# Kernel optimization log

Measured on AMD Instinct MI355X. Metric: run time of the kernel, lower is better.

Reference implementation:

```python
import jax, jax.numpy as jnp
import numpy as np
import math

INPUT_SIZE = 2048
HIDDEN_SIZE = 2048
BATCH = 4096


def setup_inputs() -> dict:
    key = jax.random.key(0)
    ks = jax.random.split(key, 16)
    stdv = 1.0 / math.sqrt(HIDDEN_SIZE)

    def u(k, shape):
        return jax.random.uniform(k, shape, jnp.float32, -stdv, stdv)

    inp = {
        "x": jax.random.normal(ks[0], (BATCH, INPUT_SIZE), jnp.float32),
        "h_x": jax.random.normal(ks[1], (BATCH, HIDDEN_SIZE), jnp.float32),
        "c_x": jax.random.normal(ks[2], (BATCH, HIDDEN_SIZE), jnp.float32),
        "W_xi": u(ks[3], (INPUT_SIZE, HIDDEN_SIZE)),
        "W_hi": u(ks[4], (HIDDEN_SIZE, HIDDEN_SIZE)),
        "b_i": u(ks[5], (HIDDEN_SIZE,)),
        "W_xf": u(ks[6], (INPUT_SIZE, HIDDEN_SIZE)),
        "W_hf": u(ks[7], (HIDDEN_SIZE, HIDDEN_SIZE)),
        "b_f": u(ks[8], (HIDDEN_SIZE,)),
        "W_xc": u(ks[9], (INPUT_SIZE, HIDDEN_SIZE)),
        "W_hc": u(ks[10], (HIDDEN_SIZE, HIDDEN_SIZE)),
        "b_c": u(ks[11], (HIDDEN_SIZE,)),
        "W_xo": u(ks[12], (INPUT_SIZE, HIDDEN_SIZE)),
        "W_ho": u(ks[13], (HIDDEN_SIZE, HIDDEN_SIZE)),
        "b_o": u(ks[14], (HIDDEN_SIZE,)),
    }
    return inp


def reference(x, h_x, c_x, W_xi, W_hi, b_i, W_xf, W_hf, b_f, W_xc, W_hc, b_c, W_xo, W_ho, b_o):
    # LSTM cell: 4 gates, each x @ W_x* + h @ W_h* + b_*
    input_gate = jax.nn.sigmoid(x @ W_xi + h_x @ W_hi + b_i)
    forget_gate = jax.nn.sigmoid(x @ W_xf + h_x @ W_hf + b_f)
    output_gate = jax.nn.sigmoid(x @ W_xo + h_x @ W_ho + b_o)
    c_tilda = jnp.tanh(x @ W_xc + h_x @ W_hc + b_c)
    cy = forget_gate * c_x + input_gate * c_tilda
    hy = output_gate * jnp.tanh(cy)
    return (hy, cy)
```

## Files before the change

kernel.cpp:

```cpp
#include <hip/hip_runtime.h>
#include <stdint.h>

typedef __attribute__((ext_vector_type(8))) short short8;
typedef __attribute__((ext_vector_type(8))) unsigned short ushort8;
typedef __attribute__((ext_vector_type(4))) float floatx4;

#define BATCH 4096
#define HID   2048
#define KTOT  4096

__device__ __forceinline__ uint16_t f2bf(float f) {
    union { uint32_t i; float f; } v; v.f = f;
    uint32_t u = v.i;
    u += 0x7fffu + ((u >> 16) & 1u);
    return (uint16_t)(u >> 16);
}
__device__ __forceinline__ float sigmoid_f(float v) {
    return 1.0f / (1.0f + __expf(-v));
}
__device__ __forceinline__ float tanh_f(float v) {
    v = fminf(fmaxf(v, -15.0f), 15.0f);
    float e = __expf(-2.0f * v);
    return (1.0f - e) / (1.0f + e);
}
__device__ __forceinline__ void load_lds16(const uint16_t* g, uint16_t* l) {
    __builtin_amdgcn_global_load_lds(
        (const __attribute__((address_space(1))) void*)g,
        (__attribute__((address_space(3))) void*)l, 16, 0, 0);
}

__global__ __launch_bounds__(256) void conv_w(
    const float* __restrict__ w0, const float* __restrict__ w1,
    const float* __restrict__ w2, const float* __restrict__ w3,
    const float* __restrict__ w4, const float* __restrict__ w5,
    const float* __restrict__ w6, const float* __restrict__ w7,
    uint16_t* __restrict__ wt)
{
    int b   = blockIdx.x;
    int mi  = b >> 8;
    int rem = b & 255;
    int k0  = (rem >> 4) * 128;
    int n0  = (rem & 15) * 128;
    const float* src;
    switch (mi) {
        case 0: src = w0; break; case 1: src = w1; break;
        case 2: src = w2; break; case 3: src = w3; break;
        case 4: src = w4; break; case 5: src = w5; break;
        case 6: src = w6; break; default: src = w7; break;
    }
    int g = mi >> 1, half = mi & 1;
    int ty = threadIdx.x >> 4, tx = threadIdx.x & 15;
    int kr = k0 + ty * 8;
    int nc = n0 + tx * 8;

    ushort8 a[8];
    #pragma unroll
    for (int j = 0; j < 8; ++j) {
        const float* s = src + (size_t)(kr + j) * HID + nc;
        floatx4 f0 = *(const floatx4*)(s);
        floatx4 f1 = *(const floatx4*)(s + 4);
        #pragma unroll
        for (int i = 0; i < 4; ++i) {
            a[j][i]     = f2bf(f0[i]);
            a[j][4 + i] = f2bf(f1[i]);
        }
    }
    ushort8 bt[8];
    #pragma unroll
    for (int i = 0; i < 8; ++i)
        #pragma unroll
        for (int j = 0; j < 8; ++j)
            bt[i][j] = a[j][i];
    #pragma unroll
    for (int i = 0; i < 8; ++i)
        *(ushort8*)(wt + ((size_t)g * HID + nc + i) * KTOT + half * HID + kr) = bt[i];
}

__global__ __launch_bounds__(256) void conv_a(
    const float* __restrict__ x, const float* __restrict__ h,
    uint16_t* __restrict__ xh)
{
    size_t base = ((size_t)blockIdx.x * 256 + threadIdx.x) * 8;
    int m = (int)(base >> 12);
    int k = (int)(base & (KTOT - 1));
    const float* s = (k < HID) ? (x + (size_t)m * HID + k)
                               : (h + (size_t)m * HID + (k - HID));
    floatx4 f0 = *(const floatx4*)(s);
    floatx4 f1 = *(const floatx4*)(s + 4);
    ushort8 v;
    #pragma unroll
    for (int j = 0; j < 4; ++j) { v[j] = f2bf(f0[j]); v[4 + j] = f2bf(f1[j]); }
    *(ushort8*)(xh + base) = v;
}

__global__ __launch_bounds__(256, 4) void lstm_gemm_bf16(
    const uint16_t* __restrict__ xh, const float* __restrict__ cx,
    const uint16_t* __restrict__ wt,
    const float* __restrict__ bvi, const float* __restrict__ bvf,
    const float* __restrict__ bvo, const float* __restrict__ bvc,
    float* __restrict__ out)
{
    __shared__ uint16_t ldsA[128 * 64];
    __shared__ uint16_t ldsB[128 * 64];

    int t = threadIdx.x;
    int linear = blockIdx.y * gridDim.x + blockIdx.x;
    int my = (linear & 7) * 4 + ((linear >> 3) & 3);
    int nx = linear >> 5;
    int n0 = nx * 32;
    int m0 = my * 128;

    int wave = t >> 6, lane = t & 63;
    int wr = wave >> 1, wc = wave & 1;
    int lrow = lane & 15, quad = lane >> 4;
    int swz  = lrow & 7;

    int srow = t >> 3;
    int schk = (t & 7) ^ (srow & 7);

    floatx4 acc[4][4] = {};

    for (int kt = 0; kt < KTOT / 64; ++kt) {
        int k0 = kt * 64;

        __syncthreads();
        #pragma unroll
        for (int p = 0; p < 4; ++p) {
            int row = srow + p * 32;
            load_lds16(xh + (size_t)(m0 + row) * KTOT + k0 + schk * 8,
                       ldsA + p * 2048 + t * 8);
        }
        #pragma unroll
        for (int p = 0; p < 4; ++p) {
            int j = srow + p * 32;
            int g = j >> 5, dn = j & 31;
            load_lds16(wt + ((size_t)g * HID + n0 + dn) * KTOT + k0 + schk * 8,
                       ldsB + p * 2048 + t * 8);
        }
        __syncthreads();

        #pragma unroll
        for (int kh = 0; kh < 2; ++kh) {
            int kkc = kh * 4;
            short8 af[4], bfr[4];
            #pragma unroll
            for (int mi = 0; mi < 4; ++mi)
                af[mi] = *(const short8*)(ldsA + (wr * 64 + mi * 16 + lrow) * 64
                                               + (((quad + kkc) ^ swz)) * 8);
            #pragma unroll
            for (int g = 0; g < 4; ++g)
                bfr[g] = *(const short8*)(ldsB + (g * 32 + wc * 16 + lrow) * 64
                                               + (((quad + kkc) ^ swz)) * 8);
            #pragma unroll
            for (int mi = 0; mi < 4; ++mi)
                #pragma unroll
                for (int g = 0; g < 4; ++g)
                    acc[mi][g] = __builtin_amdgcn_mfma_f32_16x16x32_bf16(
                        af[mi], bfr[g], acc[mi][g], 0, 0, 0);
        }
    }

    int col = n0 + wc * 16 + lrow;
    float Bi = bvi[col], Bf = bvf[col], Bo = bvo[col], Bc = bvc[col];
    int rowb = m0 + wr * 64 + quad * 4;

    #pragma unroll
    for (int mi = 0; mi < 4; ++mi) {
        #pragma unroll
        for (int r = 0; r < 4; ++r) {
            int row = rowb + mi * 16 + r;
            size_t off = (size_t)row * HID + col;
            float gi = sigmoid_f(acc[mi][0][r] + Bi);
            float gf = sigmoid_f(acc[mi][1][r] + Bf);
            float go = sigmoid_f(acc[mi][2][r] + Bo);
            float gc = tanh_f   (acc[mi][3][r] + Bc);
            float cyv = gf * cx[off] + gi * gc;
            float hyv = go * tanh_f(cyv);
            out[off] = hyv;
            out[(size_t)BATCH * HID + off] = cyv;
        }
    }
}

__global__ __launch_bounds__(256) void lstm_fused_f32(
    const float* __restrict__ x, const float* __restrict__ h,
    const float* __restrict__ cx,
    const float* __restrict__ wxi, const float* __restrict__ whi,
    const float* __restrict__ wxf, const float* __restrict__ whf,
    const float* __restrict__ wxo, const float* __restrict__ who,
    const float* __restrict__ wxc, const float* __restrict__ whc,
    const float* __restrict__ bvi, const float* __restrict__ bvf,
    const float* __restrict__ bvo, const float* __restrict__ bvc,
    float* __restrict__ out)
{
    __shared__ uint16_t ldsA[128 * 32];
    __shared__ uint16_t ldsB[128 * 32];
    uint32_t* ldsB32 = (uint32_t*)ldsB;

    int t    = threadIdx.x;
    int n0   = blockIdx.x * 32;
    int m0   = blockIdx.y * 128;
    int wave = t >> 6, lane = t & 63;
    int wr = wave >> 1, wc = wave & 1;
    int lrow = lane & 15, quad = lane >> 4;
    int srow = t >> 2;
    int sseg = (t & 3) * 8;
    int gw = wave;
    int ng = lane & 3;
    int ka = lane >> 2;
    const float *wxg, *whg;
    switch (gw) {
        case 0:  wxg = wxi; whg = whi; break;
        case 1:  wxg = wxf; whg = whf; break;
        case 2:  wxg = wxo; whg = who; break;
        default: wxg = wxc; whg = whc; break;
    }

    floatx4 acc[4][4] = {};

    for (int kt = 0; kt < KTOT / 32; ++kt) {
        int k0  = kt * 32;
        int k0h = k0 & (HID - 1);
        bool xhalf = (k0 < HID);

        ushort8 va[2];
        uint32_t bw[8];
        const float* a = xhalf ? x : h;
        #pragma unroll
        for (int p = 0; p < 2; ++p) {
            const float* s = a + (size_t)(m0 + srow + p * 64) * HID + k0h + sseg;
            floatx4 f0 = *(const floatx4*)(s);
            floatx4 f1 = *(const floatx4*)(s + 4);
            #pragma unroll
            for (int j = 0; j < 4; ++j) {
                va[p][j]     = (short)f2bf(f0[j]);
                va[p][4 + j] = (short)f2bf(f1[j]);
            }
        }
        const float* wp  = xhalf ? wxg : whg;
        const float* r0p = wp + (size_t)(k0h + 2 * ka) * HID + n0 + ng * 8;
        floatx4 a0 = *(const floatx4*)(r0p);
        floatx4 a1 = *(const floatx4*)(r0p + 4);
        floatx4 b0 = *(const floatx4*)(r0p + HID);
        floatx4 b1 = *(const floatx4*)(r0p + HID + 4);
        #pragma unroll
        for (int j = 0; j < 4; ++j) {
            bw[j]     = (uint32_t)f2bf(a0[j]) | ((uint32_t)f2bf(b0[j]) << 16);
            bw[4 + j] = (uint32_t)f2bf(a1[j]) | ((uint32_t)f2bf(b1[j]) << 16);
        }

        __syncthreads();
        #pragma unroll
        for (int p = 0; p < 2; ++p)
            *(ushort8*)(ldsA + (srow + p * 64) * 32 + sseg) = va[p];
        #pragma unroll
        for (int j = 0; j < 8; ++j)
            ldsB32[(gw * 32 + ng * 8 + j) * 16 + ka] = bw[j];
        __syncthreads();

        short8 af[4], bfr[4];
        #pragma unroll
        for (int mi = 0; mi < 4; ++mi)
            af[mi] = *(const short8*)(ldsA + (wr * 64 + mi * 16 + lrow) * 32 + quad * 8);
        #pragma unroll
        for (int g = 0; g < 4; ++g)
            bfr[g] = *(const short8*)(ldsB + (g * 32 + wc * 16 + lrow) * 32 + quad * 8);

        #pragma unroll
        for (int mi = 0; mi < 4; ++mi)
            #pragma unroll
            for (int g = 0; g < 4; ++g)
                acc[mi][g] = __builtin_amdgcn_mfma_f32_16x16x32_bf16(
                    af[mi], bfr[g], acc[mi][g], 0, 0, 0);
    }

    int col = n0 + wc * 16 + lrow;
    float Bi = bvi[col], Bf = bvf[col], Bo = bvo[col], Bc = bvc[col];
    int rowb = m0 + wr * 64 + quad * 4;

    #pragma unroll
    for (int mi = 0; mi < 4; ++mi) {
        #pragma unroll
        for (int r = 0; r < 4; ++r) {
            int row = rowb + mi * 16 + r;
            size_t off = (size_t)row * HID + col;
            float gi = sigmoid_f(acc[mi][0][r] + Bi);
            float gf = sigmoid_f(acc[mi][1][r] + Bf);
            float go = sigmoid_f(acc[mi][2][r] + Bo);
            float gc = tanh_f   (acc[mi][3][r] + Bc);
            float cyv = gf * cx[off] + gi * gc;
            float hyv = go * tanh_f(cyv);
            out[off] = hyv;
            out[(size_t)BATCH * HID + off] = cyv;
        }
    }
}

extern "C" void kernel_launch(void* const* d_in, const int* in_sizes, int n_in,
                              void* d_out, int out_size, void* d_ws, size_t ws_size,
                              hipStream_t stream) {
    const float* x    = (const float*)d_in[0];
    const float* h_x  = (const float*)d_in[1];
    const float* c_x  = (const float*)d_in[2];
    const float* W_xi = (const float*)d_in[3];
    const float* W_hi = (const float*)d_in[4];
    const float* b_i  = (const float*)d_in[5];
    const float* W_xf = (const float*)d_in[6];
    const float* W_hf = (const float*)d_in[7];
    const float* b_f  = (const float*)d_in[8];
    const float* W_xc = (const float*)d_in[9];
    const float* W_hc = (const float*)d_in[10];
    const float* b_c  = (const float*)d_in[11];
    const float* W_xo = (const float*)d_in[12];
    const float* W_ho = (const float*)d_in[13];
    const float* b_o  = (const float*)d_in[14];

    const size_t WT_BYTES = (size_t)4 * HID * KTOT * sizeof(uint16_t);
    const size_t XH_BYTES = (size_t)BATCH * KTOT * sizeof(uint16_t);

    if (ws_size >= WT_BYTES + XH_BYTES) {
        uint16_t* wt = (uint16_t*)d_ws;
        uint16_t* xh = (uint16_t*)((char*)d_ws + WT_BYTES);
        hipLaunchKernelGGL(conv_w, dim3(8 * 256), dim3(256), 0, stream,
                           W_xi, W_hi, W_xf, W_hf, W_xo, W_ho, W_xc, W_hc, wt);
        hipLaunchKernelGGL(conv_a, dim3((BATCH * KTOT) / (256 * 8)), dim3(256), 0, stream,
                           x, h_x, xh);
        hipLaunchKernelGGL(lstm_gemm_bf16, dim3(HID / 32, BATCH / 128), dim3(256), 0, stream,
                           xh, c_x, wt, b_i, b_f, b_o, b_c, (float*)d_out);
    } else {
        hipLaunchKernelGGL(lstm_fused_f32, dim3(HID / 32, BATCH / 128), dim3(256), 0, stream,
                           x, h_x, c_x,
                           W_xi, W_hi, W_xf, W_hf, W_xo, W_ho, W_xc, W_hc,
                           b_i, b_f, b_o, b_c, (float*)d_out);
    }
}
```

Measured before the change: 501.1 us.

## Double-buffer LDS with larger 256x64 tiles and 8-wave interleaved MFMA schedule

Replaces the 128x32(x4 gate) single-buffered GEMM with a 512-thread kernel computing 256 rows by 64 columns per gate. It double-buffers A/B tiles in 128KB of LDS so global-to-LDS loads for the next K tile overlap MFMA work on the current one. Explicit barriers and setprio around MFMA groups interleave the waves. The grid is remapped to a 1D XCD-aware ordering. The larger tiles raise arithmetic intensity, but LDS use limits occupancy and the hand-placed barriers add sync cost and correctness risk.

New measurement: 508.0 us. Within noise of the previous version (+1.4%).

```diff
diff --git a/kernel.cpp b/kernel.cpp
--- a/kernel.cpp
+++ b/kernel.cpp
@@ -93,79 +93,120 @@
     *(ushort8*)(xh + base) = v;
 }
 
-__global__ __launch_bounds__(256, 4) void lstm_gemm_bf16(
+
+#define MFMA16(B0_)                                                           \
+    __builtin_amdgcn_s_setprio(1);                                            \
+    _Pragma("unroll") for (int i_ = 0; i_ < 4; ++i_)                          \
+      _Pragma("unroll") for (int g_ = 0; g_ < 4; ++g_)                        \
+        acc[(B0_) + i_][g_] = __builtin_amdgcn_mfma_f32_16x16x32_bf16(        \
+            af[i_], bf[g_], acc[(B0_) + i_][g_], 0, 0, 0);                    \
+    __builtin_amdgcn_s_setprio(0);
+
+#define DO_TILE(RA, RB, SA, SB, K0S, DOSTAGE)                                 \
+  {                                                                           \
+               \
+    _Pragma("unroll") for (int g_ = 0; g_ < 4; ++g_)                          \
+      bf[g_] = *(const short8*)((RB) + g_ * 4096 + pc0e);                     \
+    _Pragma("unroll") for (int i_ = 0; i_ < 4; ++i_)                          \
+      af[i_] = *(const short8*)((RA) + i_ * 1024 + pc0e);                     \
+    if (DOSTAGE) {                                                            \
+      _Pragma("unroll") for (int p_ = 0; p_ < 4; ++p_)                        \
+        load_lds16(gA + (size_t)p_ * (64 * KTOT) + (K0S), (SA) + p_ * 4096);  \
+      _Pragma("unroll") for (int p_ = 0; p_ < 4; ++p_)                        \
+        load_lds16(gB + (size_t)p_ * ((size_t)HID * KTOT) + (K0S),            \
+                   (SB) + p_ * 4096);                                         \
+    }                                                                         \
+    __builtin_amdgcn_s_barrier();                                             \
+    MFMA16(0)                                                                 \
+    __builtin_amdgcn_s_barrier();                                             \
+                           \
+    _Pragma("unroll") for (int i_ = 0; i_ < 4; ++i_)                          \
+      af[i_] = *(const short8*)((RA) + (4 + i_) * 1024 + pc0e);               \
+    __builtin_amdgcn_s_barrier();                                             \
+    MFMA16(4)                                                                 \
+    __builtin_amdgcn_s_barrier();                                             \
+                                                 \
+    _Pragma("unroll") for (int g_ = 0; g_ < 4; ++g_)                          \
+      bf[g_] = *(const short8*)((RB) + g_ * 4096 + pc1e);                     \
+    _Pragma("unroll") for (int i_ = 0; i_ < 4; ++i_)                          \
+      af[i_] = *(const short8*)((RA) + i_ * 1024 + pc1e);                     \
+    __builtin_amdgcn_s_barrier();                                             \
+    MFMA16(0)                                                                 \
+    __builtin_amdgcn_s_barrier();                                             \
+           \
+    _Pragma("unroll") for (int i_ = 0; i_ < 4; ++i_)                          \
+      af[i_] = *(const short8*)((RA) + (4 + i_) * 1024 + pc1e);               \
+    __builtin_amdgcn_s_barrier();                                             \
+    MFMA16(4)                                                                 \
+    asm volatile("s_waitcnt vmcnt(0)" ::: "memory");                          \
+    __builtin_amdgcn_s_barrier();                                             \
+  }
+
+__global__ __launch_bounds__(512, 2) void lstm_gemm_bf16(
     const uint16_t* __restrict__ xh, const float* __restrict__ cx,
     const uint16_t* __restrict__ wt,
     const float* __restrict__ bvi, const float* __restrict__ bvf,
     const float* __restrict__ bvo, const float* __restrict__ bvc,
     float* __restrict__ out)
 {
-    __shared__ uint16_t ldsA[128 * 64];
-    __shared__ uint16_t ldsB[128 * 64];
+    __shared__ uint16_t lds[65536];
 
     int t = threadIdx.x;
-    int linear = blockIdx.y * gridDim.x + blockIdx.x;
-    int my = (linear & 7) * 4 + ((linear >> 3) & 3);
-    int nx = linear >> 5;
-    int n0 = nx * 32;
-    int m0 = my * 128;
+
+    int linear = blockIdx.x;
+    int wg = (linear & 7) * 64 + (linear >> 3);
+    int my = wg >> 5;
+    int nx = wg & 31;
+    int m0 = my * 256;
+    int n0 = nx * 64;
 
     int wave = t >> 6, lane = t & 63;
-    int wr = wave >> 1, wc = wave & 1;
+    int wr = wave >> 2, wc = wave & 3;
     int lrow = lane & 15, quad = lane >> 4;
     int swz  = lrow & 7;
 
     int srow = t >> 3;
     int schk = (t & 7) ^ (srow & 7);
-
-    floatx4 acc[4][4] = {};
-
-    for (int kt = 0; kt < KTOT / 64; ++kt) {
-        int k0 = kt * 64;
-
-        __syncthreads();
-        #pragma unroll
-        for (int p = 0; p < 4; ++p) {
-            int row = srow + p * 32;
-            load_lds16(xh + (size_t)(m0 + row) * KTOT + k0 + schk * 8,
-                       ldsA + p * 2048 + t * 8);
-        }
-        #pragma unroll
-        for (int p = 0; p < 4; ++p) {
-            int j = srow + p * 32;
-            int g = j >> 5, dn = j & 31;
-            load_lds16(wt + ((size_t)g * HID + n0 + dn) * KTOT + k0 + schk * 8,
-                       ldsB + p * 2048 + t * 8);
-        }
-        __syncthreads();
-
-        #pragma unroll
-        for (int kh = 0; kh < 2; ++kh) {
-            int kkc = kh * 4;
-            short8 af[4], bfr[4];
-            #pragma unroll
-            for (int mi = 0; mi < 4; ++mi)
-                af[mi] = *(const short8*)(ldsA + (wr * 64 + mi * 16 + lrow) * 64
-                                               + (((quad + kkc) ^ swz)) * 8);
-            #pragma unroll
-            for (int g = 0; g < 4; ++g)
-                bfr[g] = *(const short8*)(ldsB + (g * 32 + wc * 16 + lrow) * 64
-                                               + (((quad + kkc) ^ swz)) * 8);
-            #pragma unroll
-            for (int mi = 0; mi < 4; ++mi)
-                #pragma unroll
-                for (int g = 0; g < 4; ++g)
-                    acc[mi][g] = __builtin_amdgcn_mfma_f32_16x16x32_bf16(
-                        af[mi], bfr[g], acc[mi][g], 0, 0, 0);
-        }
+    const uint16_t* gA = xh + (size_t)(m0 + srow) * KTOT + (size_t)schk * 8;
+    const uint16_t* gB = wt + (size_t)(n0 + srow) * KTOT + (size_t)schk * 8;
+    uint16_t* sA0 = lds + t * 8;
+    uint16_t* sB0 = lds + 16384 + t * 8;
+    uint16_t* sA1 = lds + 32768 + t * 8;
+    uint16_t* sB1 = lds + 49152 + t * 8;
+
+    int aRow = wr * 128 + lrow;
+    int bRow = wc * 16 + lrow;
+    int pc0e = (quad ^ swz) * 8;
+    int pc1e = ((quad + 4) ^ swz) * 8;
+    const uint16_t* rA0 = lds + aRow * 64;
+    const uint16_t* rB0 = lds + 16384 + bRow * 64;
+    const uint16_t* rA1 = lds + 32768 + aRow * 64;
+    const uint16_t* rB1 = lds + 49152 + bRow * 64;
+
+    floatx4 acc[8][4] = {};
+    short8 af[4], bf[4];
+
+    #pragma unroll
+    for (int p = 0; p < 4; ++p)
+        load_lds16(gA + (size_t)p * (64 * KTOT), sA0 + p * 4096);
+    #pragma unroll
+    for (int p = 0; p < 4; ++p)
+        load_lds16(gB + (size_t)p * ((size_t)HID * KTOT), sB0 + p * 4096);
+    asm volatile("s_waitcnt vmcnt(0)" ::: "memory");
+    __builtin_amdgcn_s_barrier();
+
+    for (int it = 0; it < 32; ++it) {
+        size_t k0o = (size_t)it * 128 + 64;
+        DO_TILE(rA0, rB0, sA1, sB1, k0o, true);
+        DO_TILE(rA1, rB1, sA0, sB0, k0o + 64, it < 31);
     }
 
     int col = n0 + wc * 16 + lrow;
     float Bi = bvi[col], Bf = bvf[col], Bo = bvo[col], Bc = bvc[col];
-    int rowb = m0 + wr * 64 + quad * 4;
-
-    #pragma unroll
-    for (int mi = 0; mi < 4; ++mi) {
+    int rowb = m0 + wr * 128 + quad * 4;
+
+    #pragma unroll
+    for (int mi = 0; mi < 8; ++mi) {
         #pragma unroll
         for (int r = 0; r < 4; ++r) {
             int row = rowb + mi * 16 + r;
@@ -325,7 +366,7 @@
                            W_xi, W_hi, W_xf, W_hf, W_xo, W_ho, W_xc, W_hc, wt);
         hipLaunchKernelGGL(conv_a, dim3((BATCH * KTOT) / (256 * 8)), dim3(256), 0, stream,
                            x, h_x, xh);
-        hipLaunchKernelGGL(lstm_gemm_bf16, dim3(HID / 32, BATCH / 128), dim3(256), 0, stream,
+        hipLaunchKernelGGL(lstm_gemm_bf16, dim3((BATCH / 256) * (HID / 64)), dim3(512), 0, stream,
                            xh, c_x, wt, b_i, b_f, b_o, b_c, (float*)d_out);
     } else {
         hipLaunchKernelGGL(lstm_fused_f32, dim3(HID / 32, BATCH / 128), dim3(256), 0, stream,
```

## Merge weight and activation bf16 conversion into one kernel with LDS-staged transpose

Applied to the files above, without the earlier changes.

Replaces the separate weight-transpose and activation-conversion kernels with a single launch. Blocks below 1024 transpose 256x128 weight tiles through a swizzled LDS buffer so each row writes 128 contiguous bytes to global memory. Higher blocks convert four activation rows each. The aim is to remove one launch and the scattered 16-byte transposed stores, at the cost of a ~66KB shared tile that limits occupancy.

After: 514.1 us. 1.03x slower.

```diff
diff --git a/kernel.cpp b/kernel.cpp
--- a/kernel.cpp
+++ b/kernel.cpp
@@ -29,18 +29,42 @@
         (__attribute__((address_space(3))) void*)l, 16, 0, 0);
 }
 
-__global__ __launch_bounds__(256) void conv_w(
+__global__ __launch_bounds__(512) void conv_all(
     const float* __restrict__ w0, const float* __restrict__ w1,
     const float* __restrict__ w2, const float* __restrict__ w3,
     const float* __restrict__ w4, const float* __restrict__ w5,
     const float* __restrict__ w6, const float* __restrict__ w7,
-    uint16_t* __restrict__ wt)
+    const float* __restrict__ x,  const float* __restrict__ h,
+    uint16_t* __restrict__ wt,    uint16_t* __restrict__ xh)
 {
+    __shared__ uint16_t tile[256 * 132];
+
+    int t = threadIdx.x;
+
+    if (blockIdx.x >= 1024) {
+        int idx = blockIdx.x - 1024;
+        int m   = idx * 4 + (t >> 7);
+        int k   = (t & 127) * 32;
+        const float* s = (k < HID) ? (x + (size_t)m * HID + k)
+                                   : (h + (size_t)m * HID + (k - HID));
+        uint16_t* d = xh + (size_t)m * KTOT + k;
+        #pragma unroll
+        for (int q = 0; q < 4; ++q) {
+            floatx4 f0 = *(const floatx4*)(s + q * 8);
+            floatx4 f1 = *(const floatx4*)(s + q * 8 + 4);
+            ushort8 v;
+            #pragma unroll
+            for (int j = 0; j < 4; ++j) { v[j] = f2bf(f0[j]); v[4+j] = f2bf(f1[j]); }
+            *(ushort8*)(d + q * 8) = v;
+        }
+        return;
+    }
+
     int b   = blockIdx.x;
-    int mi  = b >> 8;
-    int rem = b & 255;
-    int k0  = (rem >> 4) * 128;
-    int n0  = (rem & 15) * 128;
+    int mi  = b >> 7;
+    int rem = b & 127;
+    int n0  = (rem >> 4) * 256;
+    int k0  = (rem & 15) * 128;
     const float* src;
     switch (mi) {
         case 0: src = w0; break; case 1: src = w1; break;
@@ -49,16 +73,15 @@
         case 6: src = w6; break; default: src = w7; break;
     }
     int g = mi >> 1, half = mi & 1;
-    int ty = threadIdx.x >> 4, tx = threadIdx.x & 15;
-    int kr = k0 + ty * 8;
-    int nc = n0 + tx * 8;
+
+    int kg = t >> 5, ng = t & 31;
+    const float* rp = src + (size_t)(k0 + kg * 8) * HID + n0 + ng * 8;
 
     ushort8 a[8];
     #pragma unroll
     for (int j = 0; j < 8; ++j) {
-        const float* s = src + (size_t)(kr + j) * HID + nc;
-        floatx4 f0 = *(const floatx4*)(s);
-        floatx4 f1 = *(const floatx4*)(s + 4);
+        floatx4 f0 = *(const floatx4*)(rp + (size_t)j * HID);
+        floatx4 f1 = *(const floatx4*)(rp + (size_t)j * HID + 4);
         #pragma unroll
         for (int i = 0; i < 4; ++i) {
             a[j][i]     = f2bf(f0[i]);
@@ -71,26 +94,23 @@
         #pragma unroll
         for (int j = 0; j < 8; ++j)
             bt[i][j] = a[j][i];
+
     #pragma unroll
     for (int i = 0; i < 8; ++i)
-        *(ushort8*)(wt + ((size_t)g * HID + nc + i) * KTOT + half * HID + kr) = bt[i];
-}
-
-__global__ __launch_bounds__(256) void conv_a(
-    const float* __restrict__ x, const float* __restrict__ h,
-    uint16_t* __restrict__ xh)
-{
-    size_t base = ((size_t)blockIdx.x * 256 + threadIdx.x) * 8;
-    int m = (int)(base >> 12);
-    int k = (int)(base & (KTOT - 1));
-    const float* s = (k < HID) ? (x + (size_t)m * HID + k)
-                               : (h + (size_t)m * HID + (k - HID));
-    floatx4 f0 = *(const floatx4*)(s);
-    floatx4 f1 = *(const floatx4*)(s + 4);
-    ushort8 v;
-    #pragma unroll
-    for (int j = 0; j < 4; ++j) { v[j] = f2bf(f0[j]); v[4 + j] = f2bf(f1[j]); }
-    *(ushort8*)(xh + base) = v;
+        *(ushort8*)(tile + (ng * 8 + i) * 132 + ((kg ^ ng) & 15) * 8) = bt[i];
+    __syncthreads();
+
+    int nl = t >> 1, hf = t & 1;
+    uint16_t* dst = wt + ((size_t)g * HID + n0 + nl) * KTOT
+                       + (size_t)half * HID + k0 + hf * 64;
+    int swr = (nl >> 3) & 15;
+    #pragma unroll
+    for (int j = 0; j < 8; ++j) {
+        int c    = hf * 8 + j;
+        int phys = (c ^ swr) & 15;
+        ushort8 v = *(const ushort8*)(tile + nl * 132 + phys * 8);
+        *(ushort8*)(dst + j * 8) = v;
+    }
 }
 
 __global__ __launch_bounds__(256, 4) void lstm_gemm_bf16(
@@ -321,10 +341,9 @@
     if (ws_size >= WT_BYTES + XH_BYTES) {
         uint16_t* wt = (uint16_t*)d_ws;
         uint16_t* xh = (uint16_t*)((char*)d_ws + WT_BYTES);
-        hipLaunchKernelGGL(conv_w, dim3(8 * 256), dim3(256), 0, stream,
-                           W_xi, W_hi, W_xf, W_hf, W_xo, W_ho, W_xc, W_hc, wt);
-        hipLaunchKernelGGL(conv_a, dim3((BATCH * KTOT) / (256 * 8)), dim3(256), 0, stream,
-                           x, h_x, xh);
+        hipLaunchKernelGGL(conv_all, dim3(2048), dim3(512), 0, stream,
+                           W_xi, W_hi, W_xf, W_hf, W_xo, W_ho, W_xc, W_hc,
+                           x, h_x, wt, xh);
         hipLaunchKernelGGL(lstm_gemm_bf16, dim3(HID / 32, BATCH / 128), dim3(256), 0, stream,
                            xh, c_x, wt, b_i, b_f, b_o, b_c, (float*)d_out);
     } else {
```
